# Optimization experiments

Measured on AMD Instinct MI355X. Metric: run time of the kernel, lower is better.

Reference implementation:

```python
import jax, jax.numpy as jnp
import numpy as np

B, L, D, H = 2, 2048, 1024, 16
d = D // H  # head dim = 64


def setup_inputs() -> dict:
    key = jax.random.key(0)
    ks = jax.random.split(key, 6)
    X = jax.random.normal(ks[0], (B, L, D), dtype=jnp.float32)
    scale = 0.02
    Wq = scale * jax.random.normal(ks[1], (D, D), dtype=jnp.float32)
    Wk = scale * jax.random.normal(ks[2], (D, D), dtype=jnp.float32)
    Wv = scale * jax.random.normal(ks[3], (D, D), dtype=jnp.float32)
    Wc = scale * jax.random.normal(ks[4], (D, D), dtype=jnp.float32)
    Ltri = scale * jax.random.normal(ks[5], (H, d, d), dtype=jnp.float32)
    return {"X": X, "Wq": Wq, "Wk": Wk, "Wv": Wv, "Wc": Wc, "Ltri": Ltri}


def reference(X, Wq, Wk, Wv, Wc, Ltri):
    # torch nn.Linear: y = x @ W.T (bias=False); dropout is identity in eval.
    Bsz, Lq, Dm = X.shape
    Q = (X @ Wq.T).reshape(Bsz, Lq, H, d)
    K = (X @ Wk.T).reshape(Bsz, Lq, H, d)
    V = (X @ Wv.T).reshape(Bsz, Lq, H, d)
    # Causal linear attention: cumulative sum of per-position K outer V.
    # W[b,l,h,:,:] = sum_{t<=l} K[b,t,h,:] outer V[b,t,h,:]
    KV = jnp.einsum('blhd,blhe->blhde', K, V)  # [B,L,H,d,d]
    KVc = jnp.cumsum(KV, axis=1)
    Y = jnp.einsum('blhd,blhde->blhe', Q, KVc)  # [B,L,H,d]
    # Learned SPD head-mixing matrix Bm = Lm @ Lm.T with Lm lower-triangular.
    mask = jnp.tril(jnp.ones((1, d, d), dtype=X.dtype))
    Lm = Ltri * mask  # [H,d,d]
    Bm = Lm @ jnp.swapaxes(Lm, -2, -1)  # [H,d,d]
    Y = jnp.einsum('hed,blhd->blhe', Bm, Y)
    Y = Y.reshape(Bsz, Lq, Dm)
    return Y @ Wc.T
```

## Files before the change

### kernel.cpp

```cpp
#include <hip/hip_runtime.h>


#define DEV static __device__ __forceinline__

typedef unsigned short u16;
typedef unsigned long long u64;
typedef __attribute__((ext_vector_type(4))) float f32x4;
typedef __attribute__((ext_vector_type(8))) short bf16x8;

DEV u16 f2bf(float f){
  union { float f; unsigned u; } v; v.f = f;
  unsigned r = v.u + 0x7FFFu + ((v.u >> 16) & 1u);
  return (u16)(r >> 16);
}

DEV void store_val(float* p, float v){ *p = v; }
DEV void store_val(u16* p, float v){ *p = f2bf(v); }

DEV void gload16(const void* g, void* l){
  __builtin_amdgcn_global_load_lds((const __attribute__((address_space(1))) void*)g,
                                   (__attribute__((address_space(3))) void*)l, 16, 0, 0);
}

__global__ __launch_bounds__(256) void prep_kernel(
    const float* __restrict__ X, u16* __restrict__ Xb,
    const float* __restrict__ Wq, u16* __restrict__ Wqb,
    const float* __restrict__ Wk, u16* __restrict__ Wkb,
    const float* __restrict__ Wv, u16* __restrict__ Wvb,
    const float* __restrict__ Wc, u16* __restrict__ Wcb,
    const float* __restrict__ Ltri, u16* __restrict__ Bmb)
{
  const int bx = blockIdx.x, tid = threadIdx.x;
  if(bx < 16){
    __shared__ float Lm[64][65];
    int h = bx;
    const float* src = Ltri + (size_t)h * 4096;
    for(int i = tid; i < 4096; i += 256){
      int e = i >> 6, k = i & 63;
      Lm[e][k] = (k <= e) ? src[i] : 0.f;
    }
    __syncthreads();
    u16* out = Bmb + (size_t)h * 4096;
    for(int i = tid; i < 4096; i += 256){
      int e = i >> 6, dk = i & 63;
      float sum = 0.f;
      int kmax = e < dk ? e : dk;
      for(int k = 0; k <= kmax; k++) sum += Lm[e][k] * Lm[dk][k];
      out[i] = f2bf(sum);
    }
  } else {
    const int n0 = 4194304, n1 = 1048576, n2 = 1048576, n3 = 1048576, n4 = 1048576;
    int total = (n0 + n1 + n2 + n3 + n4) >> 2;
    for(int i = (bx - 16) * 256 + tid; i < total; i += 2048 * 256){
      int e = i << 2;
      const float* s; u16* d;
      if(e < n0){ s = X + e; d = Xb + e; }
      else if(e < n0 + n1){ s = Wq + (e - n0); d = Wqb + (e - n0); }
      else if(e < n0 + n1 + n2){ s = Wk + (e - n0 - n1); d = Wkb + (e - n0 - n1); }
      else if(e < n0 + n1 + n2 + n3){ s = Wv + (e - n0 - n1 - n2); d = Wvb + (e - n0 - n1 - n2); }
      else { s = Wc + (e - n0 - n1 - n2 - n3); d = Wcb + (e - n0 - n1 - n2 - n3); }
      float4 v = *(const float4*)s;
      u64 pk = (u64)f2bf(v.x) | ((u64)f2bf(v.y) << 16) | ((u64)f2bf(v.z) << 32) | ((u64)f2bf(v.w) << 48);
      *(u64*)d = pk;
    }
  }
}

template<typename OutT>
DEV void gemm128_p2(const u16* __restrict__ A, const u16* __restrict__ W,
                    OutT* __restrict__ C, int bx, int by, int N, int K)
{
  __shared__ u16 L[3][8192];
  const int tid = threadIdx.x;
  const int wid = tid >> 6, lane = tid & 63;
  const int wr = wid >> 1, wc = wid & 1;
  const int lr = lane & 15, lq = lane >> 4;
  const u16* Ag = A + (size_t)(bx * 128) * K;
  const u16* Wg = W + (size_t)(by * 128) * K;

  const int p0 = tid >> 3, p1 = 32 + (tid >> 3);
  const int cl0 = (tid & 7) ^ (p0 & 7);
  const int cl1 = (tid & 7) ^ (p1 & 7);
  const int srow0 = 2 * p0 + (cl0 >> 2), skc0 = (cl0 & 3) * 8;
  const int srow1 = 2 * p1 + (cl1 >> 2), skc1 = (cl1 & 3) * 8;

  auto stagef = [&](int kt, int buf){
    gload16(Ag + (size_t)srow0 * K + kt * 32 + skc0, &L[buf][tid * 8]);
    gload16(Ag + (size_t)srow1 * K + kt * 32 + skc1, &L[buf][2048 + tid * 8]);
    gload16(Wg + (size_t)srow0 * K + kt * 32 + skc0, &L[buf][4096 + tid * 8]);
    gload16(Wg + (size_t)srow1 * K + kt * 32 + skc1, &L[buf][6144 + tid * 8]);
  };

  const int nt = K >> 5;
  f32x4 acc[4][4] = {};
  stagef(0, 0);
  stagef(1, 1);
  int cur = 0;
  for(int t = 0; t < nt; t++){
    if(t < nt - 1) asm volatile("s_waitcnt vmcnt(4)" ::: "memory");
    else           asm volatile("s_waitcnt vmcnt(0)" ::: "memory");
    __builtin_amdgcn_s_barrier();
    __builtin_amdgcn_sched_barrier(0);
    if(t + 2 < nt){
      int n2 = cur >= 1 ? cur - 1 : cur + 2;
      stagef(t + 2, n2);
    }
    const u16* Lb = L[cur];
    bf16x8 af[4], bfr[4];
#pragma unroll
    for(int i = 0; i < 4; i++){
      int row = wr * 64 + i * 16 + lr;
      int rh = row >> 1;
      int cph = (lq | ((row & 1) << 2)) ^ (rh & 7);
      af[i] = *(const bf16x8*)&Lb[rh * 64 + cph * 8];
    }
#pragma unroll
    for(int j = 0; j < 4; j++){
      int row = wc * 64 + j * 16 + lr;
      int rh = row >> 1;
      int cph = (lq | ((row & 1) << 2)) ^ (rh & 7);
      bfr[j] = *(const bf16x8*)&Lb[4096 + rh * 64 + cph * 8];
    }
#pragma unroll
    for(int i = 0; i < 4; i++)
#pragma unroll
      for(int j = 0; j < 4; j++)
        acc[i][j] = __builtin_amdgcn_mfma_f32_16x16x32_bf16(af[i], bfr[j], acc[i][j], 0, 0, 0);
    cur = cur == 2 ? 0 : cur + 1;
  }
#pragma unroll
  for(int i = 0; i < 4; i++)
#pragma unroll
    for(int j = 0; j < 4; j++)
#pragma unroll
      for(int r = 0; r < 4; r++){
        int row = bx * 128 + wr * 64 + i * 16 + (lane >> 4) * 4 + r;
        int col = by * 128 + wc * 64 + j * 16 + lr;
        store_val(C + (size_t)row * N + col, acc[i][j][r]);
      }
}

__global__ __launch_bounds__(256) void qkv_gemm(
    const u16* __restrict__ Xb,
    const u16* __restrict__ Wq, const u16* __restrict__ Wk, const u16* __restrict__ Wv,
    u16* __restrict__ Q, u16* __restrict__ Ko, u16* __restrict__ V,
    const u16* __restrict__ Wcb, const u16* __restrict__ Bmb, u16* __restrict__ Wcpb)
{
  if(blockIdx.y >= 24){
    int rt = blockIdx.x & 7, h = (blockIdx.x >> 3) + ((blockIdx.y - 24) << 2);
    int wid = threadIdx.x >> 6, lane = threadIdx.x & 63;
    int lr = lane & 15, lk8 = (lane >> 4) * 8, lq = lane >> 4;
    const u16* ab  = Wcb + (size_t)(rt * 128) * 1024 + h * 64;
    const u16* bm  = Bmb + (size_t)h * 4096;
    f32x4 acc[2][4] = {};
#pragma unroll
    for(int i = 0; i < 2; i++){
      int mf = wid * 2 + i;
#pragma unroll
      for(int ks = 0; ks < 2; ks++){
        bf16x8 a = *(const bf16x8*)(ab + (size_t)(mf * 16 + lr) * 1024 + ks * 32 + lk8);
#pragma unroll
        for(int nf = 0; nf < 4; nf++){
          bf16x8 bfr = *(const bf16x8*)(bm + (nf * 16 + lr) * 64 + ks * 32 + lk8);
          acc[i][nf] = __builtin_amdgcn_mfma_f32_16x16x32_bf16(a, bfr, acc[i][nf], 0, 0, 0);
        }
      }
    }
#pragma unroll
    for(int i = 0; i < 2; i++)
#pragma unroll
      for(int nf = 0; nf < 4; nf++)
#pragma unroll
        for(int r = 0; r < 4; r++){
          int row = rt * 128 + (wid * 2 + i) * 16 + lq * 4 + r;
          int col = h * 64 + nf * 16 + lr;
          Wcpb[(size_t)row * 1024 + col] = f2bf(acc[i][nf][r]);
        }
    return;
  }
  int id = blockIdx.y * 32 + blockIdx.x;
  int id2 = (id & 7) * 96 + (id >> 3);
  int bxg = id2 & 31, byg = id2 >> 5;
  int sel = byg >> 3, byl = byg & 7;
  const u16* W = sel == 0 ? Wq : sel == 1 ? Wk : Wv;
  u16* C = sel == 0 ? Q : sel == 1 ? Ko : V;
  gemm128_p2<u16>(Xb, W, C, bxg, byl, 1024, 1024);
}

__global__ __launch_bounds__(256) void out_gemm(
    const u16* __restrict__ Yb, const u16* __restrict__ Wcpb, float* __restrict__ out)
{
  int id = blockIdx.y * 32 + blockIdx.x;
  int id2 = (id & 7) * 32 + (id >> 3);
  gemm128_p2<float>(Yb, Wcpb, out, id2 & 31, id2 >> 5, 1024, 1024);
}

__global__ __launch_bounds__(256) void state_chunk(
    const u16* __restrict__ Kb, const u16* __restrict__ Vb,
    u16* __restrict__ VT, float* __restrict__ Sc)
{
  int bh = blockIdx.x, c = blockIdx.y;
  int b = bh >> 4, h = bh & 15;
  int tid = threadIdx.x;
  __shared__ u16 Kt[128][72];
  __shared__ u16 Vt[128][72];
  int rr = tid >> 3;
  int cc = (tid & 7) * 8;
  const u16* kg = Kb + (size_t)(b * 2048 + c * 128) * 1024 + h * 64;
  const u16* vg = Vb + (size_t)(b * 2048 + c * 128) * 1024 + h * 64;
#pragma unroll
  for(int p = 0; p < 4; p++){
    int row = rr + p * 32;
    *(int4*)&Kt[row][cc] = *(const int4*)(kg + (size_t)row * 1024 + cc);
    *(int4*)&Vt[row][cc] = *(const int4*)(vg + (size_t)row * 1024 + cc);
  }
  __syncthreads();
  {
    int d = tid >> 2, tseg = (tid & 3) * 32;
    u16* vto = VT + (size_t)bh * 64 * 2048 + (size_t)d * 2048 + c * 128 + tseg;
#pragma unroll
    for(int j = 0; j < 32; j += 8){
      u16 tmp[8] __attribute__((aligned(16)));
#pragma unroll
      for(int q = 0; q < 8; q++) tmp[q] = Vt[tseg + j + q][d];
      *(int4*)(vto + j) = *(const int4*)tmp;
    }
  }
  int wid = tid >> 6, lane = tid & 63;
  int wr = wid >> 1, wc = wid & 1;
  int lr = lane & 15, lk8 = (lane >> 4) * 8, lq = lane >> 4;
  f32x4 acc[2][2] = {};
#pragma unroll
  for(int ks = 0; ks < 4; ks++){
    bf16x8 a[2], bb[2];
#pragma unroll
    for(int i = 0; i < 2; i++){
      u16 tmp[8] __attribute__((aligned(16)));
      int e = wr * 32 + i * 16 + lr;
#pragma unroll
      for(int q = 0; q < 8; q++) tmp[q] = Vt[ks * 32 + lk8 + q][e];
      a[i] = *(const bf16x8*)tmp;
    }
#pragma unroll
    for(int j = 0; j < 2; j++){
      u16 tmp[8] __attribute__((aligned(16)));
      int dk = wc * 32 + j * 16 + lr;
#pragma unroll
      for(int q = 0; q < 8; q++) tmp[q] = Kt[ks * 32 + lk8 + q][dk];
      bb[j] = *(const bf16x8*)tmp;
    }
#pragma unroll
    for(int i = 0; i < 2; i++)
#pragma unroll
      for(int j = 0; j < 2; j++)
        acc[i][j] = __builtin_amdgcn_mfma_f32_16x16x32_bf16(a[i], bb[j], acc[i][j], 0, 0, 0);
  }
  float* out = Sc + ((size_t)bh * 16 + c) * 4096;
#pragma unroll
  for(int i = 0; i < 2; i++)
#pragma unroll
    for(int j = 0; j < 2; j++)
#pragma unroll
      for(int r = 0; r < 4; r++){
        int e = wr * 32 + i * 16 + lq * 4 + r, dk = wc * 32 + j * 16 + lr;
        out[e * 64 + dk] = acc[i][j][r];
      }
}

__global__ __launch_bounds__(256) void prefix_state(const float* __restrict__ Sc, u16* __restrict__ Scb)
{
  int bh = blockIdx.x >> 2, part = blockIdx.x & 3;
  int e4 = part * 256 + threadIdx.x;
  const float4* s = (const float4*)(Sc + (size_t)bh * 65536) + e4;
  u16* d = Scb + (size_t)bh * 65536 + e4 * 4;
  float4 run = {0.f, 0.f, 0.f, 0.f};
  for(int c = 0; c < 16; c++){
    float4 v = s[(size_t)c * 1024];
    u64 pk = (u64)f2bf(run.x) | ((u64)f2bf(run.y) << 16) | ((u64)f2bf(run.z) << 32) | ((u64)f2bf(run.w) << 48);
    *(u64*)(d + (size_t)c * 4096) = pk;
    run.x += v.x; run.y += v.y; run.z += v.z; run.w += v.w;
  }
}

__global__ __launch_bounds__(256) void chunk_attn(
    const u16* __restrict__ Q, const u16* __restrict__ Kmat,
    const u16* __restrict__ VT, const u16* __restrict__ Scb, u16* __restrict__ Y)
{
  int bh = blockIdx.x, c = blockIdx.y;
  int b = bh >> 4, h = bh & 15;
  int t = threadIdx.x, wid = t >> 6, lane = t & 63;
  int lr = lane & 15, lk8 = (lane >> 4) * 8, lq = lane >> 4;
  __shared__ u16 S[128 * 128];
  const u16* qg = Q    + (size_t)(b * 2048 + c * 128) * 1024 + h * 64;
  const u16* kg = Kmat + (size_t)(b * 2048 + c * 128) * 1024 + h * 64;
  const u16* scb = Scb + ((size_t)bh * 16 + c) * 4096;
  const u16* vt  = VT + (size_t)bh * 64 * 2048 + (size_t)c * 128;
  u16* yg = Y + (size_t)(b * 2048 + c * 128) * 1024 + h * 64;

  bf16x8 a[2][2];
#pragma unroll
  for(int mi = 0; mi < 2; mi++){
    int mf = wid + mi * 4;
    int Rm = mf * 16;
    if((mf & 1) == 0){
      int zr = Rm + (lane >> 2), zc = Rm + 16 + (lane & 3) * 4;
      int zoff = ((zr * 128 + zc) * 2) ^ ((zr & 7) << 4);
      *(u64*)((char*)S + zoff) = 0ULL;
    }
#pragma unroll
    for(int ks = 0; ks < 2; ks++) a[mi][ks] = *(const bf16x8*)(qg + (size_t)(Rm + lr) * 1024 + ks * 32 + lk8);
    for(int nf = 0; nf <= mf; nf++){
      f32x4 acc = {};
#pragma unroll
      for(int ks = 0; ks < 2; ks++){
        bf16x8 bb = *(const bf16x8*)(kg + (size_t)(nf * 16 + lr) * 1024 + ks * 32 + lk8);
        acc = __builtin_amdgcn_mfma_f32_16x16x32_bf16(a[mi][ks], bb, acc, 0, 0, 0);
      }
#pragma unroll
      for(int r = 0; r < 4; r++){
        int row = lq * 4 + r, col = lr;
        float v = acc[r];
        if(nf == mf && col > row) v = 0.f;
        int grow = Rm + row, gcol = nf * 16 + col;
        int off = ((grow * 128 + gcol) * 2) ^ ((grow & 7) << 4);
        *(u16*)((char*)S + off) = f2bf(v);
      }
    }
  }
  f32x4 acc2[2][4] = {};
#pragma unroll
  for(int nf = 0; nf < 4; nf++)
#pragma unroll
    for(int ks = 0; ks < 2; ks++){
      bf16x8 bb = *(const bf16x8*)(scb + (nf * 16 + lr) * 64 + ks * 32 + lk8);
#pragma unroll
      for(int mi = 0; mi < 2; mi++)
        acc2[mi][nf] = __builtin_amdgcn_mfma_f32_16x16x32_bf16(a[mi][ks], bb, acc2[mi][nf], 0, 0, 0);
    }
  int ks0 = wid >> 1;
  int row0 = wid * 16 + lr;
  int row1 = (wid + 4) * 16 + lr;
  for(int ks = 0; ks <= ks0 + 2; ks++){
    bf16x8 bb[4];
#pragma unroll
    for(int nf = 0; nf < 4; nf++)
      bb[nf] = *(const bf16x8*)(vt + (size_t)(nf * 16 + lr) * 2048 + ks * 32 + lk8);
    if(ks <= ks0){
      int off = ((row0 * 128 + ks * 32 + lk8) * 2) ^ ((row0 & 7) << 4);
      bf16x8 af = *(const bf16x8*)((char*)S + off);
#pragma unroll
      for(int nf = 0; nf < 4; nf++)
        acc2[0][nf] = __builtin_amdgcn_mfma_f32_16x16x32_bf16(af, bb[nf], acc2[0][nf], 0, 0, 0);
    }
    {
      int off = ((row1 * 128 + ks * 32 + lk8) * 2) ^ ((row1 & 7) << 4);
      bf16x8 af = *(const bf16x8*)((char*)S + off);
#pragma unroll
      for(int nf = 0; nf < 4; nf++)
        acc2[1][nf] = __builtin_amdgcn_mfma_f32_16x16x32_bf16(af, bb[nf], acc2[1][nf], 0, 0, 0);
    }
  }
#pragma unroll
  for(int mi = 0; mi < 2; mi++){
    int Rm = (wid + mi * 4) * 16;
#pragma unroll
    for(int nf = 0; nf < 4; nf++)
#pragma unroll
      for(int r = 0; r < 4; r++){
        int grow = Rm + lq * 4 + r, gcol = nf * 16 + lr;
        yg[(size_t)grow * 1024 + gcol] = f2bf(acc2[mi][nf][r]);
      }
  }
}

extern "C" void kernel_launch(void* const* d_in, const int* in_sizes, int n_in,
                              void* d_out, int out_size, void* d_ws, size_t ws_size,
                              hipStream_t stream)
{
  const float* X    = (const float*)d_in[0];
  const float* Wq   = (const float*)d_in[1];
  const float* Wk   = (const float*)d_in[2];
  const float* Wv   = (const float*)d_in[3];
  const float* Wc   = (const float*)d_in[4];
  const float* Ltri = (const float*)d_in[5];
  float* out = (float*)d_out;

  char* ws = (char*)d_ws;
  size_t off = 0;
  auto carve = [&](size_t bytes) -> char* {
    char* p = ws + off;
    off += (bytes + 255) & ~(size_t)255;
    return p;
  };
  u16* Xb   = (u16*)carve((size_t)4194304 * 2);
  u16* Wqb  = (u16*)carve((size_t)1048576 * 2);
  u16* Wkb  = (u16*)carve((size_t)1048576 * 2);
  u16* Wvb  = (u16*)carve((size_t)1048576 * 2);
  u16* Wcb  = (u16*)carve((size_t)1048576 * 2);
  u16* Wcpb = (u16*)carve((size_t)1048576 * 2);
  u16* Bmb  = (u16*)carve((size_t)65536 * 2);
  u16* Qb   = (u16*)carve((size_t)4194304 * 2);
  u16* Kb   = (u16*)carve((size_t)4194304 * 2);
  u16* Vb   = (u16*)carve((size_t)4194304 * 2);
  u16* VT   = (u16*)carve((size_t)4194304 * 2);
  float* Sc = (float*)carve((size_t)2097152 * 4);
  u16* Scb  = (u16*)carve((size_t)2097152 * 2);
  u16* Yb   = (u16*)carve((size_t)4194304 * 2);
  (void)in_sizes; (void)n_in; (void)out_size; (void)ws_size;

  prep_kernel<<<2064, 256, 0, stream>>>(X, Xb, Wq, Wqb, Wk, Wkb, Wv, Wvb, Wc, Wcb, Ltri, Bmb);
  qkv_gemm<<<dim3(32, 28), 256, 0, stream>>>(Xb, Wqb, Wkb, Wvb, Qb, Kb, Vb, Wcb, Bmb, Wcpb);
  state_chunk<<<dim3(32, 16), 256, 0, stream>>>(Kb, Vb, VT, Sc);
  prefix_state<<<128, 256, 0, stream>>>(Sc, Scb);
  chunk_attn<<<dim3(32, 16), 256, 0, stream>>>(Qb, Kb, VT, Scb, Yb);
  out_gemm<<<dim3(32, 8), 256, 0, stream>>>(Yb, Wcpb, out);
}
```

Baseline: 107.8 us.

## Add swizzled 4-buffer GEMM for output projection and transpose K/V in LDS

Adds a new GEMM variant with four LDS stages, three loads in flight, XOR-swizzled LDS layout and explicit vmcnt waits, and uses it for the output projection. The qkv and out GEMMs also drop their block-ID remapping and use plain blockIdx, which changes L2 locality. The state_chunk kernel now transposes K and V once into separate LDS tiles, so MFMA operands come from single vector loads instead of eight scalar strided reads. This costs extra LDS space and one more barrier.

Measured after the change: 106.0 us. Within noise of the previous version (-1.6%).

```diff
diff --git a/kernel.cpp b/kernel.cpp
--- a/kernel.cpp
+++ b/kernel.cpp
@@ -140,6 +140,77 @@
       }
 }
 
+template<typename OutT>
+DEV void gemm128_p3(const u16* __restrict__ A, const u16* __restrict__ W,
+                    OutT* __restrict__ C, int bx, int by, int N, int K)
+{
+  __shared__ u16 L[4][8192];
+  const int tid = threadIdx.x;
+  const int wid = tid >> 6, lane = tid & 63;
+  const int wr = wid >> 1, wc = wid & 1;
+  const int lr = lane & 15, lq = lane >> 4;
+  const u16* Ag = A + (size_t)(bx * 128) * K;
+  const u16* Wg = W + (size_t)(by * 128) * K;
+
+  const int p0 = tid >> 3, p1 = 32 + (tid >> 3);
+  const int cl0 = (tid & 7) ^ (p0 & 7);
+  const int cl1 = (tid & 7) ^ (p1 & 7);
+  const int srow0 = 2 * p0 + (cl0 >> 2), skc0 = (cl0 & 3) * 8;
+  const int srow1 = 2 * p1 + (cl1 >> 2), skc1 = (cl1 & 3) * 8;
+
+  auto stagef = [&](int kt, int buf){
+    gload16(Ag + (size_t)srow0 * K + kt * 32 + skc0, &L[buf][tid * 8]);
+    gload16(Ag + (size_t)srow1 * K + kt * 32 + skc1, &L[buf][2048 + tid * 8]);
+    gload16(Wg + (size_t)srow0 * K + kt * 32 + skc0, &L[buf][4096 + tid * 8]);
+    gload16(Wg + (size_t)srow1 * K + kt * 32 + skc1, &L[buf][6144 + tid * 8]);
+  };
+
+  const int nt = K >> 5;
+  f32x4 acc[4][4] = {};
+  stagef(0, 0);
+  stagef(1, 1);
+  stagef(2, 2);
+  for(int t = 0; t < nt; t++){
+    if(t < nt - 2)       asm volatile("s_waitcnt vmcnt(8)" ::: "memory");
+    else if(t == nt - 2) asm volatile("s_waitcnt vmcnt(4)" ::: "memory");
+    else                 asm volatile("s_waitcnt vmcnt(0)" ::: "memory");
+    __builtin_amdgcn_s_barrier();
+    __builtin_amdgcn_sched_barrier(0);
+    if(t + 3 < nt) stagef(t + 3, (t + 3) & 3);
+    const u16* Lb = L[t & 3];
+    bf16x8 af[4], bfr[4];
+#pragma unroll
+    for(int i = 0; i < 4; i++){
+      int row = wr * 64 + i * 16 + lr;
+      int rh = row >> 1;
+      int cph = (lq | ((row & 1) << 2)) ^ (rh & 7);
+      af[i] = *(const bf16x8*)&Lb[rh * 64 + cph * 8];
+    }
+#pragma unroll
+    for(int j = 0; j < 4; j++){
+      int row = wc * 64 + j * 16 + lr;
+      int rh = row >> 1;
+      int cph = (lq | ((row & 1) << 2)) ^ (rh & 7);
+      bfr[j] = *(const bf16x8*)&Lb[4096 + rh * 64 + cph * 8];
+    }
+#pragma unroll
+    for(int i = 0; i < 4; i++)
+#pragma unroll
+      for(int j = 0; j < 4; j++)
+        acc[i][j] = __builtin_amdgcn_mfma_f32_16x16x32_bf16(af[i], bfr[j], acc[i][j], 0, 0, 0);
+  }
+#pragma unroll
+  for(int i = 0; i < 4; i++)
+#pragma unroll
+    for(int j = 0; j < 4; j++)
+#pragma unroll
+      for(int r = 0; r < 4; r++){
+        int row = bx * 128 + wr * 64 + i * 16 + (lane >> 4) * 4 + r;
+        int col = by * 128 + wc * 64 + j * 16 + lr;
+        store_val(C + (size_t)row * N + col, acc[i][j][r]);
+      }
+}
+
 __global__ __launch_bounds__(256) void qkv_gemm(
     const u16* __restrict__ Xb,
     const u16* __restrict__ Wq, const u16* __restrict__ Wk, const u16* __restrict__ Wv,
@@ -178,21 +249,16 @@
         }
     return;
   }
-  int id = blockIdx.y * 32 + blockIdx.x;
-  int id2 = (id & 7) * 96 + (id >> 3);
-  int bxg = id2 & 31, byg = id2 >> 5;
-  int sel = byg >> 3, byl = byg & 7;
+  int sel = blockIdx.y >> 3, byl = blockIdx.y & 7;
   const u16* W = sel == 0 ? Wq : sel == 1 ? Wk : Wv;
   u16* C = sel == 0 ? Q : sel == 1 ? Ko : V;
-  gemm128_p2<u16>(Xb, W, C, bxg, byl, 1024, 1024);
+  gemm128_p2<u16>(Xb, W, C, blockIdx.x, byl, 1024, 1024);
 }
 
 __global__ __launch_bounds__(256) void out_gemm(
     const u16* __restrict__ Yb, const u16* __restrict__ Wcpb, float* __restrict__ out)
 {
-  int id = blockIdx.y * 32 + blockIdx.x;
-  int id2 = (id & 7) * 32 + (id >> 3);
-  gemm128_p2<float>(Yb, Wcpb, out, id2 & 31, id2 >> 5, 1024, 1024);
+  gemm128_p3<float>(Yb, Wcpb, out, blockIdx.x, blockIdx.y, 1024, 1024);
 }
 
 __global__ __launch_bounds__(256) void state_chunk(
@@ -204,6 +270,8 @@
   int tid = threadIdx.x;
   __shared__ u16 Kt[128][72];
   __shared__ u16 Vt[128][72];
+  __shared__ u16 KtT[64][136];
+  __shared__ u16 VtT[64][136];
   int rr = tid >> 3;
   int cc = (tid & 7) * 8;
   const u16* kg = Kb + (size_t)(b * 2048 + c * 128) * 1024 + h * 64;
@@ -215,16 +283,25 @@
     *(int4*)&Vt[row][cc] = *(const int4*)(vg + (size_t)row * 1024 + cc);
   }
   __syncthreads();
+  int d = tid >> 2, tseg = (tid & 3) * 32;
+#pragma unroll
+  for(int j = 0; j < 32; j += 8){
+    u16 tk[8] __attribute__((aligned(16)));
+    u16 tv[8] __attribute__((aligned(16)));
+#pragma unroll
+    for(int q = 0; q < 8; q++){
+      tk[q] = Kt[tseg + j + q][d];
+      tv[q] = Vt[tseg + j + q][d];
+    }
+    *(int4*)&KtT[d][tseg + j] = *(const int4*)tk;
+    *(int4*)&VtT[d][tseg + j] = *(const int4*)tv;
+  }
+  __syncthreads();
   {
-    int d = tid >> 2, tseg = (tid & 3) * 32;
     u16* vto = VT + (size_t)bh * 64 * 2048 + (size_t)d * 2048 + c * 128 + tseg;
 #pragma unroll
-    for(int j = 0; j < 32; j += 8){
-      u16 tmp[8] __attribute__((aligned(16)));
-#pragma unroll
-      for(int q = 0; q < 8; q++) tmp[q] = Vt[tseg + j + q][d];
-      *(int4*)(vto + j) = *(const int4*)tmp;
-    }
+    for(int j = 0; j < 32; j += 8)
+      *(int4*)(vto + j) = *(const int4*)&VtT[d][tseg + j];
   }
   int wid = tid >> 6, lane = tid & 63;
   int wr = wid >> 1, wc = wid & 1;
@@ -234,21 +311,9 @@
   for(int ks = 0; ks < 4; ks++){
     bf16x8 a[2], bb[2];
 #pragma unroll
-    for(int i = 0; i < 2; i++){
-      u16 tmp[8] __attribute__((aligned(16)));
-      int e = wr * 32 + i * 16 + lr;
-#pragma unroll
-      for(int q = 0; q < 8; q++) tmp[q] = Vt[ks * 32 + lk8 + q][e];
-      a[i] = *(const bf16x8*)tmp;
-    }
-#pragma unroll
-    for(int j = 0; j < 2; j++){
-      u16 tmp[8] __attribute__((aligned(16)));
-      int dk = wc * 32 + j * 16 + lr;
-#pragma unroll
-      for(int q = 0; q < 8; q++) tmp[q] = Kt[ks * 32 + lk8 + q][dk];
-      bb[j] = *(const bf16x8*)tmp;
-    }
+    for(int i = 0; i < 2; i++) a[i]  = *(const bf16x8*)&VtT[wr * 32 + i * 16 + lr][ks * 32 + lk8];
+#pragma unroll
+    for(int j = 0; j < 2; j++) bb[j] = *(const bf16x8*)&KtT[wc * 32 + j * 16 + lr][ks * 32 + lk8];
 #pragma unroll
     for(int i = 0; i < 2; i++)
 #pragma unroll
```
